# Optimization experiments

Hardware: AMD Instinct MI355X
Metric: run time of the kernel (lower is better)

Reference implementation:

```python
import jax, jax.numpy as jnp
import numpy as np

B, D, ML = 16384, 256, 10
EPS = 1e-6


def setup_inputs() -> dict:
    key = jax.random.key(0)
    ks = jax.random.split(key, 20)
    s = 0.02
    return {
        "O_t": jax.random.normal(ks[0], (B, D), jnp.float32),
        "O_prev": jax.random.normal(ks[1], (B, D), jnp.float32),
        "memory": jax.random.normal(ks[2], (B, ML, D), jnp.float32),
        # weight_mlp: Linear(3 -> D) (see notes re: source bug) + Tanh
        "w_mlp_W": jax.random.normal(ks[3], (D, 3), jnp.float32) * s,
        "w_mlp_b": jnp.zeros((D,), jnp.float32),
        # single-step LSTM (input 2D -> hidden D), torch gate order i,f,g,o
        "lstm_Wih": jax.random.normal(ks[4], (4 * D, 2 * D), jnp.float32) * s,
        "lstm_Whh": jax.random.normal(ks[5], (4 * D, D), jnp.float32) * s,
        "lstm_bih": jnp.zeros((4 * D,), jnp.float32),
        "lstm_bhh": jnp.zeros((4 * D,), jnp.float32),
        "q_W": jax.random.normal(ks[6], (D, D), jnp.float32) * s,
        "q_b": jnp.zeros((D,), jnp.float32),
        "k_W": jax.random.normal(ks[7], (D, D), jnp.float32) * s,
        "k_b": jnp.zeros((D,), jnp.float32),
        "v_W": jax.random.normal(ks[8], (D, D), jnp.float32) * s,
        "v_b": jnp.zeros((D,), jnp.float32),
        "z_W": jax.random.normal(ks[9], (D, 2 * D), jnp.float32) * s,
        "z_b": jnp.zeros((D,), jnp.float32),
        "r_W": jax.random.normal(ks[10], (D, 2 * D), jnp.float32) * s,
        "r_b": jnp.zeros((D,), jnp.float32),
        "h_W": jax.random.normal(ks[11], (D, 2 * D), jnp.float32) * s,
        "h_b": jnp.zeros((D,), jnp.float32),
    }


def _dltc(O_t, O_prev, memory, w_mlp_W, w_mlp_b, lstm_Wih, lstm_Whh,
          lstm_bih, lstm_bhh, q_W, q_b, k_W, k_b, v_W, v_b,
          z_W, z_b, r_W, r_b, h_W, h_b):
    d = O_t.shape[1]
    # --- dynamic frame weighting ---
    n_t = jnp.linalg.norm(O_t, axis=1, keepdims=True)            # [B,1]
    n_p = jnp.linalg.norm(O_prev, axis=1, keepdims=True)         # [B,1]
    rho_delta = jnp.linalg.norm(O_t - O_prev, axis=1, keepdims=True)
    rho_assoc = jnp.sum(O_t * O_prev, axis=1, keepdims=True) / (n_t * n_p + EPS)
    wi = jnp.concatenate([n_t, rho_delta, rho_assoc], axis=1)    # [B,3]
    W_t = (jnp.tanh(wi @ w_mlp_W.T + w_mlp_b) + 1.0) * 0.5       # [B,D]
    O_t_weighted = O_t * W_t
    # --- single-step LSTM with h0=c0=0 ---
    x = jnp.concatenate([O_prev, O_t_weighted], axis=1)          # [B,2D]
    gates = x @ lstm_Wih.T + lstm_bih + lstm_bhh                 # h0=0 => no Whh term
    i_g, f_g, g_g, o_g = jnp.split(gates, 4, axis=1)
    c = jax.nn.sigmoid(i_g) * jnp.tanh(g_g)                      # f*c0 = 0
    O_t_prime = jax.nn.sigmoid(o_g) * jnp.tanh(c)                # [B,D]
    # --- tiny attention over memory ---
    Q = O_t_prime @ q_W.T + q_b                                  # [B,D]
    K = memory @ k_W.T + k_b                                     # [B,M,D]
    V = memory @ v_W.T + v_b
    scores = jnp.einsum('bd,bmd->bm', Q, K) / jnp.sqrt(jnp.float32(d))
    attn = jax.nn.softmax(scores, axis=-1)                       # [B,M]
    O_up = jnp.einsum('bm,bmd->bd', attn, V)                     # [B,D]
    # --- GRU-style gated memory update ---
    O_up_b = jnp.broadcast_to(O_up[:, None, :], memory.shape)    # [B,M,D]
    mem_cat = jnp.concatenate([memory, O_up_b], axis=2)          # [B,M,2D]
    z_t = jax.nn.sigmoid(mem_cat @ z_W.T + z_b)
    r_t = jax.nn.sigmoid(mem_cat @ r_W.T + r_b)
    m_tilde = jnp.tanh(jnp.concatenate([r_t * memory, O_up_b], axis=2) @ h_W.T + h_b)
    memory_new = z_t * memory + (1.0 - z_t) * m_tilde
    memory_new = jnp.concatenate([memory_new[:, 1:], O_up[:, None, :]], axis=1)
    return O_up, memory_new, O_up, W_t


def reference(O_t, O_prev, memory, w_mlp_W, w_mlp_b, lstm_Wih, lstm_Whh,
              lstm_bih, lstm_bhh, q_W, q_b, k_W, k_b, v_W, v_b,
              z_W, z_b, r_W, r_b, h_W, h_b):
    return _dltc(O_t, O_prev, memory, w_mlp_W, w_mlp_b, lstm_Wih, lstm_Whh,
                 lstm_bih, lstm_bhh, q_W, q_b, k_W, k_b, v_W, v_b,
                 z_W, z_b, r_W, r_b, h_W, h_b)
```

## Files before the change

kernel.cpp:

```cpp
#include <hip/hip_runtime.h>

#define BB 16384
#define DD 256

typedef _Float16 f16;
typedef _Float16 h8 __attribute__((ext_vector_type(8)));
typedef float v4f __attribute__((ext_vector_type(4)));

#define MFMA(a,b,c) __builtin_amdgcn_mfma_f32_16x16x32_f16((a),(b),(c),0,0,0)

__device__ __forceinline__ float sigm(float x){ return 1.0f/(1.0f + __expf(-x)); }
__device__ __forceinline__ float tanh_f(float x){ float e = __expf(2.0f*x); return 1.0f - 2.0f/(e + 1.0f); }

__device__ __forceinline__ h8 ldsA(const f16* s, int row, int stride, int k0){
  int g = (k0 >> 3) ^ (row & 7);
  return *reinterpret_cast<const h8*>(s + row*stride + g*8);
}

__global__ __launch_bounds__(512) void k0_convert(
    const float* __restrict__ Wih, const float* __restrict__ vW,
    const float* __restrict__ zW, const float* __restrict__ rW, const float* __restrict__ hW,
    f16* __restrict__ wih16, f16* __restrict__ wv16, f16* __restrict__ w2,
    f16* __restrict__ wzr1, f16* __restrict__ wh1)
{
  int idx = blockIdx.x*512 + threadIdx.x;
  if (idx < 393216){
    int j = idx >> 9, k = idx & 511;
    int sj = (j < 256) ? j : j + 256;
    wih16[idx] = (f16)Wih[sj*512 + k];
    return;
  }
  idx -= 393216;
  if (idx < 65536){ wv16[idx] = (f16)vW[idx]; return; }
  idx -= 65536;
  if (idx < 196608){
    int j = idx >> 8, k = idx & 255;
    float v = (j < 256) ? zW[j*512 + 256 + k]
            : (j < 512) ? rW[(j-256)*512 + 256 + k]
                        : hW[(j-512)*512 + 256 + k];
    w2[idx] = (f16)v;
    return;
  }
  idx -= 196608;
  if (idx < 131072){
    int j = idx >> 8, k = idx & 255;
    wzr1[idx] = (f16)((j < 256) ? zW[j*512 + k] : rW[(j-256)*512 + k]);
    return;
  }
  idx -= 131072;
  {
    int j = idx >> 8, k = idx & 255;
    wh1[idx] = (f16)hW[j*512 + k];
  }
}

__global__ __launch_bounds__(256) void k0_wqkt(const float* __restrict__ qW, const float* __restrict__ kW,
                                               f16* __restrict__ wqkt)
{
  int d = blockIdx.x, e = threadIdx.x;
  float acc = 0.f;
  for (int j = 0; j < 256; ++j) acc += qW[j*256 + e] * kW[j*256 + d];
  wqkt[d*256 + e] = (f16)acc;
}

__global__ __launch_bounds__(256) void k0_misc(const float* __restrict__ qW, const float* __restrict__ kW,
                                               const float* __restrict__ qb, const float* __restrict__ kb,
                                               float* __restrict__ bqk, float* __restrict__ u, float* __restrict__ c0)
{
  int e = threadIdx.x;
  float a = 0.f, b = 0.f;
  for (int j = 0; j < 256; ++j){ a += qb[j]*kW[j*256 + e]; b += kb[j]*qW[j*256 + e]; }
  bqk[e] = a; u[e] = b;
  if (e == 0){ float c = 0.f; for (int j = 0; j < 256; ++j) c += qb[j]*kb[j]; c0[0] = c; }
}

__global__ __launch_bounds__(512) void k1_frontend(
    const float* __restrict__ O_t, const float* __restrict__ O_prev,
    const float* __restrict__ mlpW, const float* __restrict__ mlpB,
    const float* __restrict__ bih, const float* __restrict__ bhh,
    const f16* __restrict__ wih16, const f16* __restrict__ wqkt,
    const float* __restrict__ bqk, const float* __restrict__ u, const float* __restrict__ c0,
    float* __restrict__ wt_out, float* __restrict__ Qk, float* __restrict__ sQ)
{
  __shared__ f16 xs[32*512];
  __shared__ f16 o1[32*256];
  const int t   = threadIdx.x;
  const int b0  = blockIdx.x * 32;
  const int r   = t >> 4, sub = t & 15;
  const int b   = b0 + r;

  {
    float ot[16], op[16];
    float stt = 0.f, spp = 0.f, stp = 0.f;
    const float* pt = O_t    + b*DD + sub*16;
    const float* pp = O_prev + b*DD + sub*16;
#pragma unroll
    for (int i = 0; i < 4; ++i){
      float4 a = *reinterpret_cast<const float4*>(pt + i*4);
      float4 c = *reinterpret_cast<const float4*>(pp + i*4);
      ot[i*4+0]=a.x; ot[i*4+1]=a.y; ot[i*4+2]=a.z; ot[i*4+3]=a.w;
      op[i*4+0]=c.x; op[i*4+1]=c.y; op[i*4+2]=c.z; op[i*4+3]=c.w;
      stt += a.x*a.x + a.y*a.y + a.z*a.z + a.w*a.w;
      spp += c.x*c.x + c.y*c.y + c.z*c.z + c.w*c.w;
      stp += a.x*c.x + a.y*c.y + a.z*c.z + a.w*c.w;
    }
#pragma unroll
    for (int off = 8; off >= 1; off >>= 1){
      stt += __shfl_xor(stt, off);
      spp += __shfl_xor(spp, off);
      stp += __shfl_xor(stp, off);
    }
    float n_t = sqrtf(stt), n_p = sqrtf(spp);
    float r_d = sqrtf(fmaxf(stt - 2.f*stp + spp, 0.f));
    float r_a = stp / (n_t*n_p + 1e-6f);

    h8 h0, h1;
#pragma unroll
    for (int j = 0; j < 8; ++j){ h0[j] = (f16)op[j]; h1[j] = (f16)op[8+j]; }
    *reinterpret_cast<h8*>(&xs[r*512 + (((sub*2  ) ^ (r&7)))*8]) = h0;
    *reinterpret_cast<h8*>(&xs[r*512 + (((sub*2+1) ^ (r&7)))*8]) = h1;

    float wts[16];
#pragma unroll
    for (int i = 0; i < 16; ++i){
      int d = sub*16 + i;
      float xv = mlpW[d*3+0]*n_t + mlpW[d*3+1]*r_d + mlpW[d*3+2]*r_a + mlpB[d];
      wts[i] = 0.5f*(tanh_f(xv) + 1.0f);
    }
#pragma unroll
    for (int i = 0; i < 16; i += 4){
      float4 v; v.x=wts[i]; v.y=wts[i+1]; v.z=wts[i+2]; v.w=wts[i+3];
      *reinterpret_cast<float4*>(wt_out + (size_t)b*DD + sub*16 + i) = v;
    }
    h8 u0, u1;
#pragma unroll
    for (int j = 0; j < 8; ++j){ u0[j] = (f16)(ot[j]*wts[j]); u1[j] = (f16)(ot[8+j]*wts[8+j]); }
    *reinterpret_cast<h8*>(&xs[r*512 + (((32 + sub*2  ) ^ (r&7)))*8]) = u0;
    *reinterpret_cast<h8*>(&xs[r*512 + (((32 + sub*2+1) ^ (r&7)))*8]) = u1;
  }
  __syncthreads();

  const int w = t >> 6, l = t & 63;
  const int lr = l & 15, lk = l >> 4;

  {
    v4f acc[3][2][2];
#pragma unroll
    for (int g = 0; g < 3; ++g)
#pragma unroll
      for (int dt = 0; dt < 2; ++dt)
#pragma unroll
        for (int mt = 0; mt < 2; ++mt) acc[g][dt][mt] = (v4f){0.f,0.f,0.f,0.f};

    for (int ks = 0; ks < 16; ++ks){
      h8 A0 = ldsA(xs, lr,      512, ks*32 + lk*8);
      h8 A1 = ldsA(xs, 16 + lr, 512, ks*32 + lk*8);
#pragma unroll
      for (int dt = 0; dt < 2; ++dt){
        const int dbase = (w*2 + dt)*16;
#pragma unroll
        for (int g = 0; g < 3; ++g){
          const int jrow = g*256 + dbase + lr;
          h8 Bf = *reinterpret_cast<const h8*>(wih16 + jrow*512 + ks*32 + lk*8);
          acc[g][dt][0] = MFMA(A0, Bf, acc[g][dt][0]);
          acc[g][dt][1] = MFMA(A1, Bf, acc[g][dt][1]);
        }
      }
    }
#pragma unroll
    for (int dt = 0; dt < 2; ++dt){
      const int d  = (w*2 + dt)*16 + lr;
      const float bi = bih[d]       + bhh[d];
      const float bg = bih[512 + d] + bhh[512 + d];
      const float bo = bih[768 + d] + bhh[768 + d];
#pragma unroll
      for (int mt = 0; mt < 2; ++mt){
#pragma unroll
        for (int q = 0; q < 4; ++q){
          const int row = mt*16 + lk*4 + q;
          float iv = sigm(acc[0][dt][mt][q] + bi);
          float gv = tanh_f(acc[1][dt][mt][q] + bg);
          float ov = sigm(acc[2][dt][mt][q] + bo);
          float o  = ov * tanh_f(iv*gv);
          int g = ((d >> 3) ^ (row & 7));
          o1[row*256 + g*8 + (d & 7)] = (f16)o;
        }
      }
    }
  }
  __syncthreads();

  {
    float s = 0.f;
#pragma unroll
    for (int i = 0; i < 16; ++i){
      int dd = sub*16 + i;
      int g = ((dd >> 3) ^ (r & 7));
      s += (float)o1[r*256 + g*8 + (dd & 7)] * u[dd];
    }
#pragma unroll
    for (int off = 8; off >= 1; off >>= 1) s += __shfl_xor(s, off);
    if (sub == 0) sQ[b] = s + c0[0];
  }

  {
    v4f acc[2][2];
#pragma unroll
    for (int nt = 0; nt < 2; ++nt)
#pragma unroll
      for (int mt = 0; mt < 2; ++mt) acc[nt][mt] = (v4f){0.f,0.f,0.f,0.f};

    for (int ks = 0; ks < 8; ++ks){
      h8 A0 = ldsA(o1, lr,      256, ks*32 + lk*8);
      h8 A1 = ldsA(o1, 16 + lr, 256, ks*32 + lk*8);
#pragma unroll
      for (int nt = 0; nt < 2; ++nt){
        const int dcol = (w*2 + nt)*16 + lr;
        h8 Bf = *reinterpret_cast<const h8*>(wqkt + dcol*256 + ks*32 + lk*8);
        acc[nt][0] = MFMA(A0, Bf, acc[nt][0]);
        acc[nt][1] = MFMA(A1, Bf, acc[nt][1]);
      }
    }
#pragma unroll
    for (int nt = 0; nt < 2; ++nt){
      const int dcol = (w*2 + nt)*16 + lr;
      const float bq = bqk[dcol];
#pragma unroll
      for (int mt = 0; mt < 2; ++mt){
#pragma unroll
        for (int q = 0; q < 4; ++q){
          const int row = mt*16 + lk*4 + q;
          Qk[(size_t)(b0 + row)*DD + dcol] = acc[nt][mt][q] + bq;
        }
      }
    }
  }
}

__global__ __launch_bounds__(512) void k2a_attn(
    const float* __restrict__ mem, const float* __restrict__ Qk, const float* __restrict__ sQ,
    const f16* __restrict__ wv16, const float* __restrict__ v_b,
    const f16* __restrict__ w2, float* __restrict__ out, f16* __restrict__ z2r2h2)
{
  extern __shared__ char smem[];
  f16*   ms     = (f16*)  (smem);
  float* qks    = (float*)(smem + 81920);
  float* scores = (float*)(smem + 98304);
  float* attns  = (float*)(smem + 98944);
  f16*   mbar   = (f16*)  (smem + 99584);
  f16*   oup    = (f16*)  (smem + 107776);

  const int t  = threadIdx.x;
  const int b0 = blockIdx.x * 16;
  const int sub = t & 15;

  {
    const float4* src = reinterpret_cast<const float4*>(Qk + (size_t)b0*DD);
    float4* dst = reinterpret_cast<float4*>(qks);
    dst[t] = src[t];
    dst[t + 512] = src[t + 512];
  }
  __syncthreads();

  for (int p = 0; p < 5; ++p){
    const int rl = p*32 + (t >> 4);
    const int bl = rl / 10;
    const float* srcp = mem + ((size_t)(b0*10 + rl))*DD + sub*16;
    const float* qrow = qks + bl*DD + sub*16;
    float s = 0.f;
    f16 hv[16];
#pragma unroll
    for (int i = 0; i < 4; ++i){
      float4 v = *reinterpret_cast<const float4*>(srcp + i*4);
      float4 q = *reinterpret_cast<const float4*>(qrow + i*4);
      s += v.x*q.x + v.y*q.y + v.z*q.z + v.w*q.w;
      hv[i*4+0]=(f16)v.x; hv[i*4+1]=(f16)v.y; hv[i*4+2]=(f16)v.z; hv[i*4+3]=(f16)v.w;
    }
    h8 h0, h1;
#pragma unroll
    for (int j = 0; j < 8; ++j){ h0[j]=hv[j]; h1[j]=hv[8+j]; }
    *reinterpret_cast<h8*>(&ms[rl*256 + (((sub*2  ) ^ (rl&7)))*8]) = h0;
    *reinterpret_cast<h8*>(&ms[rl*256 + (((sub*2+1) ^ (rl&7)))*8]) = h1;
#pragma unroll
    for (int off = 8; off >= 1; off >>= 1) s += __shfl_xor(s, off);
    if (sub == 0) scores[rl] = s;
  }
  __syncthreads();

  if (t < 16){
    const float sq = sQ[b0 + t];
    float e[10]; float mx = -1e30f;
#pragma unroll
    for (int m = 0; m < 10; ++m){ e[m] = (scores[t*10 + m] + sq)*0.0625f; mx = fmaxf(mx, e[m]); }
    float ss = 0.f;
#pragma unroll
    for (int m = 0; m < 10; ++m){ e[m] = __expf(e[m] - mx); ss += e[m]; }
    float inv = 1.f/ss;
#pragma unroll
    for (int m = 0; m < 10; ++m) attns[t*10 + m] = e[m]*inv;
  }
  __syncthreads();

  {
    const int rr = t >> 5;
    const int s5 = t & 31;
    float a[8];
#pragma unroll
    for (int i = 0; i < 8; ++i) a[i] = 0.f;
#pragma unroll
    for (int m = 0; m < 10; ++m){
      const int row = rr*10 + m;
      const float wg = attns[row];
      h8 h = *reinterpret_cast<const h8*>(&ms[row*256 + ((s5 ^ (row&7)))*8]);
#pragma unroll
      for (int i = 0; i < 8; ++i) a[i] += wg*(float)h[i];
    }
    h8 hb;
#pragma unroll
    for (int i = 0; i < 8; ++i) hb[i] = (f16)a[i];
    *reinterpret_cast<h8*>(&mbar[rr*256 + ((s5 ^ (rr&7)))*8]) = hb;
  }
  __syncthreads();

  const int w = t >> 6, l = t & 63, lr = l & 15, lk = l >> 4;

  {
    v4f acc[2]; acc[0] = (v4f){0.f,0.f,0.f,0.f}; acc[1] = (v4f){0.f,0.f,0.f,0.f};
    for (int ks = 0; ks < 8; ++ks){
      h8 A = ldsA(mbar, lr, 256, ks*32 + lk*8);
#pragma unroll
      for (int nt = 0; nt < 2; ++nt){
        const int col = (w*2 + nt)*16 + lr;
        h8 Bf = *reinterpret_cast<const h8*>(wv16 + col*256 + ks*32 + lk*8);
        acc[nt] = MFMA(A, Bf, acc[nt]);
      }
    }
#pragma unroll
    for (int nt = 0; nt < 2; ++nt){
      const int col = (w*2 + nt)*16 + lr;
      const float vb = v_b[col];
#pragma unroll
      for (int q = 0; q < 4; ++q){
        const int row = lk*4 + q;
        const int bb = b0 + row;
        float v = acc[nt][q] + vb;
        out[(size_t)bb*DD + col] = v;
        out[(size_t)11*BB*DD + (size_t)bb*DD + col] = v;
        out[(size_t)BB*DD + ((size_t)bb*10 + 9)*DD + col] = v;
        int g = ((col >> 3) ^ (row & 7));
        oup[row*256 + g*8 + (col & 7)] = (f16)v;
      }
    }
  }
  __syncthreads();

  {
    v4f acc[6];
#pragma unroll
    for (int j = 0; j < 6; ++j) acc[j] = (v4f){0.f,0.f,0.f,0.f};
    for (int ks = 0; ks < 8; ++ks){
      h8 A = ldsA(oup, lr, 256, ks*32 + lk*8);
#pragma unroll
      for (int j = 0; j < 6; ++j){
        const int ntg = w*6 + j;
        h8 Bf = *reinterpret_cast<const h8*>(w2 + (ntg*16 + lr)*256 + ks*32 + lk*8);
        acc[j] = MFMA(A, Bf, acc[j]);
      }
    }
#pragma unroll
    for (int j = 0; j < 6; ++j){
      const int colg = (w*6 + j)*16 + lr;
#pragma unroll
      for (int q = 0; q < 4; ++q){
        const int row = lk*4 + q;
        z2r2h2[((size_t)(b0 + row))*768 + colg] = (f16)acc[j][q];
      }
    }
  }
}

__global__ __launch_bounds__(512) void k2b_update(
    const float* __restrict__ mem, const f16* __restrict__ wzr1, const f16* __restrict__ wh1,
    const f16* __restrict__ z2r2h2, const float* __restrict__ z_b, const float* __restrict__ r_b,
    const float* __restrict__ h_b, float* __restrict__ out1)
{
  extern __shared__ char smem[];
  f16* ms = (f16*)smem;
  f16* a2 = (f16*)(smem + 40960);

  const int t  = threadIdx.x;
  const int b0 = blockIdx.x * 8;
  const int sub = t & 15;

  for (int p = 0; p < 3; ++p){
    const int rl = p*32 + (t >> 4);
    if (rl < 80){
      const float* srcp = mem + ((size_t)(b0*10 + rl))*DD + sub*16;
      f16 hv[16];
#pragma unroll
      for (int i = 0; i < 4; ++i){
        float4 v = *reinterpret_cast<const float4*>(srcp + i*4);
        hv[i*4+0]=(f16)v.x; hv[i*4+1]=(f16)v.y; hv[i*4+2]=(f16)v.z; hv[i*4+3]=(f16)v.w;
      }
      h8 h0, h1;
#pragma unroll
      for (int j = 0; j < 8; ++j){ h0[j]=hv[j]; h1[j]=hv[8+j]; }
      *reinterpret_cast<h8*>(&ms[rl*256 + (((sub*2  ) ^ (rl&7)))*8]) = h0;
      *reinterpret_cast<h8*>(&ms[rl*256 + (((sub*2+1) ^ (rl&7)))*8]) = h1;
    }
  }
  __syncthreads();

  const int w = t >> 6, l = t & 63, lr = l & 15, lk = l >> 4;
  float zreg[5][2][4];

  {
    v4f acc[5][2];
#pragma unroll
    for (int mt = 0; mt < 5; ++mt){ acc[mt][0]=(v4f){0.f,0.f,0.f,0.f}; acc[mt][1]=(v4f){0.f,0.f,0.f,0.f}; }
    for (int ks = 0; ks < 8; ++ks){
      h8 A[5];
#pragma unroll
      for (int mt = 0; mt < 5; ++mt) A[mt] = ldsA(ms, mt*16 + lr, 256, ks*32 + lk*8);
#pragma unroll
      for (int nt = 0; nt < 2; ++nt){
        const int jrow = (w*2 + nt)*16 + lr;
        h8 Bf = *reinterpret_cast<const h8*>(wzr1 + jrow*256 + ks*32 + lk*8);
#pragma unroll
        for (int mt = 0; mt < 5; ++mt) acc[mt][nt] = MFMA(A[mt], Bf, acc[mt][nt]);
      }
    }
#pragma unroll
    for (int mt = 0; mt < 5; ++mt)
#pragma unroll
      for (int nt = 0; nt < 2; ++nt){
        const int col = (w*2 + nt)*16 + lr;
#pragma unroll
        for (int q = 0; q < 4; ++q){
          const int row = mt*16 + lk*4 + q;
          const int bb = b0 + row/10;
          float x = acc[mt][nt][q] + (float)z2r2h2[(size_t)bb*768 + col] + z_b[col];
          zreg[mt][nt][q] = sigm(x);
        }
      }
  }

  {
    v4f acc[5][2];
#pragma unroll
    for (int mt = 0; mt < 5; ++mt){ acc[mt][0]=(v4f){0.f,0.f,0.f,0.f}; acc[mt][1]=(v4f){0.f,0.f,0.f,0.f}; }
    for (int ks = 0; ks < 8; ++ks){
      h8 A[5];
#pragma unroll
      for (int mt = 0; mt < 5; ++mt) A[mt] = ldsA(ms, mt*16 + lr, 256, ks*32 + lk*8);
#pragma unroll
      for (int nt = 0; nt < 2; ++nt){
        const int jrow = 256 + (w*2 + nt)*16 + lr;
        h8 Bf = *reinterpret_cast<const h8*>(wzr1 + jrow*256 + ks*32 + lk*8);
#pragma unroll
        for (int mt = 0; mt < 5; ++mt) acc[mt][nt] = MFMA(A[mt], Bf, acc[mt][nt]);
      }
    }
#pragma unroll
    for (int mt = 0; mt < 5; ++mt)
#pragma unroll
      for (int nt = 0; nt < 2; ++nt){
        const int col = (w*2 + nt)*16 + lr;
#pragma unroll
        for (int q = 0; q < 4; ++q){
          const int row = mt*16 + lk*4 + q;
          const int bb = b0 + row/10;
          float x = acc[mt][nt][q] + (float)z2r2h2[(size_t)bb*768 + 256 + col] + r_b[col];
          float rv = sigm(x);
          int g = ((col >> 3) ^ (row & 7));
          float mv = (float)ms[row*256 + g*8 + (col & 7)];
          a2[row*256 + g*8 + (col & 7)] = (f16)(rv*mv);
        }
      }
  }
  __syncthreads();

  {
    v4f acc[5][2];
#pragma unroll
    for (int mt = 0; mt < 5; ++mt){ acc[mt][0]=(v4f){0.f,0.f,0.f,0.f}; acc[mt][1]=(v4f){0.f,0.f,0.f,0.f}; }
    for (int ks = 0; ks < 8; ++ks){
      h8 A[5];
#pragma unroll
      for (int mt = 0; mt < 5; ++mt) A[mt] = ldsA(a2, mt*16 + lr, 256, ks*32 + lk*8);
#pragma unroll
      for (int nt = 0; nt < 2; ++nt){
        const int jrow = (w*2 + nt)*16 + lr;
        h8 Bf = *reinterpret_cast<const h8*>(wh1 + jrow*256 + ks*32 + lk*8);
#pragma unroll
        for (int mt = 0; mt < 5; ++mt) acc[mt][nt] = MFMA(A[mt], Bf, acc[mt][nt]);
      }
    }
#pragma unroll
    for (int mt = 0; mt < 5; ++mt)
#pragma unroll
      for (int nt = 0; nt < 2; ++nt){
        const int col = (w*2 + nt)*16 + lr;
#pragma unroll
        for (int q = 0; q < 4; ++q){
          const int row = mt*16 + lk*4 + q;
          const int bl = row/10;
          const int m  = row - bl*10;
          const int bb = b0 + bl;
          float mtld = tanh_f(acc[mt][nt][q] + (float)z2r2h2[(size_t)bb*768 + 512 + col] + h_b[col]);
          int g = ((col >> 3) ^ (row & 7));
          float mv = (float)ms[row*256 + g*8 + (col & 7)];
          float z = zreg[mt][nt][q];
          float res = z*mv + (1.f - z)*mtld;
          if (m > 0) out1[((size_t)bb*10 + (m-1))*DD + col] = res;
        }
      }
  }
}

extern "C" void kernel_launch(void* const* d_in, const int* in_sizes, int n_in,
                              void* d_out, int out_size, void* d_ws, size_t ws_size,
                              hipStream_t stream)
{
  (void)in_sizes; (void)n_in; (void)out_size; (void)ws_size;

  const float* O_t    = (const float*)d_in[0];
  const float* O_prev = (const float*)d_in[1];
  const float* mem    = (const float*)d_in[2];
  const float* mlpW   = (const float*)d_in[3];
  const float* mlpB   = (const float*)d_in[4];
  const float* Wih    = (const float*)d_in[5];
  const float* bih    = (const float*)d_in[7];
  const float* bhh    = (const float*)d_in[8];
  const float* qW     = (const float*)d_in[9];
  const float* qb     = (const float*)d_in[10];
  const float* kW     = (const float*)d_in[11];
  const float* kb     = (const float*)d_in[12];
  const float* vW     = (const float*)d_in[13];
  const float* vb     = (const float*)d_in[14];
  const float* zW     = (const float*)d_in[15];
  const float* zb     = (const float*)d_in[16];
  const float* rW     = (const float*)d_in[17];
  const float* rb     = (const float*)d_in[18];
  const float* hW     = (const float*)d_in[19];
  const float* hb     = (const float*)d_in[20];

  char* ws = (char*)d_ws;
  f16*   wih16 = (f16*)  (ws + 0);
  f16*   wqkt  = (f16*)  (ws + 786432);
  f16*   wv16  = (f16*)  (ws + 917504);
  f16*   w2    = (f16*)  (ws + 1048576);
  f16*   wzr1  = (f16*)  (ws + 1441792);
  f16*   wh1   = (f16*)  (ws + 1703936);
  float* bqk   = (float*)(ws + 1835008);
  float* u     = (float*)(ws + 1836032);
  float* c0    = (float*)(ws + 1837056);
  float* Qk    = (float*)(ws + 2097152);
  float* sQ    = (float*)(ws + 18874368);
  f16*   z2r2h2= (f16*)  (ws + 18939904);

  float* out    = (float*)d_out;
  float* wt_out = out + (size_t)12*BB*DD;
  float* out1   = out + (size_t)BB*DD;

  hipFuncSetAttribute((const void*)k2a_attn,  hipFuncAttributeMaxDynamicSharedMemorySize, 116224);
  hipFuncSetAttribute((const void*)k2b_update, hipFuncAttributeMaxDynamicSharedMemorySize, 81920);

  k0_convert<<<dim3(1664), dim3(512), 0, stream>>>(Wih, vW, zW, rW, hW, wih16, wv16, w2, wzr1, wh1);
  k0_wqkt  <<<dim3(256),  dim3(256), 0, stream>>>(qW, kW, wqkt);
  k0_misc  <<<dim3(1),    dim3(256), 0, stream>>>(qW, kW, qb, kb, bqk, u, c0);
  k1_frontend<<<dim3(512), dim3(512), 0, stream>>>(O_t, O_prev, mlpW, mlpB, bih, bhh,
                                                   wih16, wqkt, bqk, u, c0, wt_out, Qk, sQ);
  k2a_attn <<<dim3(1024), dim3(512), 116224, stream>>>(mem, Qk, sQ, wv16, vb, w2, out, z2r2h2);
  k2b_update<<<dim3(2048), dim3(512), 81920, stream>>>(mem, wzr1, wh1, z2r2h2, zb, rb, hb, out1);
}
```

Baseline: 879.8 us.

## Fuse attention and GRU memory update into one pipelined kernel

Merges the attention kernel and the gated-update kernel into a single kernel. Each block handles four groups of 8 batches, double-buffering the fp16 memory tile in LDS and prefetching the next group's memory rows into registers while computing. This removes the second read of the large memory tensor and the z2r2h2 global round trip. Outputs are staged through LDS for coalesced float4 stores, and a few inner loops are fully unrolled. The cost is higher LDS use per block (about 152KB), which limits occupancy, plus heavy register pressure from the prefetch buffers and accumulators, and fewer blocks overall.

```diff
diff --git a/kernel.cpp b/kernel.cpp
--- a/kernel.cpp
+++ b/kernel.cpp
@@ -2,6 +2,8 @@
 
 #define BB 16384
 #define DD 256
+#define GPB 4
+#define TBG 8
 
 typedef _Float16 f16;
 typedef _Float16 h8 __attribute__((ext_vector_type(8)));
@@ -15,6 +17,13 @@
 __device__ __forceinline__ h8 ldsA(const f16* s, int row, int stride, int k0){
   int g = (k0 >> 3) ^ (row & 7);
   return *reinterpret_cast<const h8*>(s + row*stride + g*8);
+}
+
+__device__ __forceinline__ void bar_lds(){
+  __builtin_amdgcn_sched_barrier(0);
+  asm volatile("s_waitcnt lgkmcnt(0)" ::: "memory");
+  __builtin_amdgcn_s_barrier();
+  __builtin_amdgcn_sched_barrier(0);
 }
 
 __global__ __launch_bounds__(512) void k0_convert(
@@ -152,6 +161,7 @@
 #pragma unroll
         for (int mt = 0; mt < 2; ++mt) acc[g][dt][mt] = (v4f){0.f,0.f,0.f,0.f};
 
+#pragma unroll
     for (int ks = 0; ks < 16; ++ks){
       h8 A0 = ldsA(xs, lr,      512, ks*32 + lk*8);
       h8 A1 = ldsA(xs, 16 + lr, 512, ks*32 + lk*8);
@@ -210,6 +220,7 @@
 #pragma unroll
       for (int mt = 0; mt < 2; ++mt) acc[nt][mt] = (v4f){0.f,0.f,0.f,0.f};
 
+#pragma unroll
     for (int ks = 0; ks < 8; ++ks){
       h8 A0 = ldsA(o1, lr,      256, ks*32 + lk*8);
       h8 A1 = ldsA(o1, 16 + lr, 256, ks*32 + lk*8);
@@ -237,284 +248,344 @@
   }
 }
 
-__global__ __launch_bounds__(512) void k2a_attn(
+
+__device__ __forceinline__ void issue_grp(float4* pf, const float* __restrict__ mem, int gb0, int t){
+  const float* basep = mem + (size_t)gb0*10*DD;
+  {
+    const float* p = basep + (t>>4)*DD + (t&15)*16;
+    pf[0] = reinterpret_cast<const float4*>(p)[0];
+    pf[1] = reinterpret_cast<const float4*>(p)[1];
+    pf[2] = reinterpret_cast<const float4*>(p)[2];
+    pf[3] = reinterpret_cast<const float4*>(p)[3];
+  }
+  {
+    const int s = t + 512;
+    const float* p = basep + (s>>4)*DD + (s&15)*16;
+    pf[4] = reinterpret_cast<const float4*>(p)[0];
+    pf[5] = reinterpret_cast<const float4*>(p)[1];
+    pf[6] = reinterpret_cast<const float4*>(p)[2];
+    pf[7] = reinterpret_cast<const float4*>(p)[3];
+  }
+  if (t < 256){
+    const int s = t + 1024;
+    const float* p = basep + (s>>4)*DD + (s&15)*16;
+    pf[8]  = reinterpret_cast<const float4*>(p)[0];
+    pf[9]  = reinterpret_cast<const float4*>(p)[1];
+    pf[10] = reinterpret_cast<const float4*>(p)[2];
+    pf[11] = reinterpret_cast<const float4*>(p)[3];
+  }
+}
+
+__device__ __forceinline__ void conv_slot(f16* __restrict__ buf, const float4* pf, int s,
+    const float* __restrict__ Qk, int gb0, float* __restrict__ scoresL)
+{
+  const int rl = s >> 4, cs = s & 15;
+  const float* qrow = Qk + (size_t)(gb0 + rl/10)*DD + cs*16;
+  float sum = 0.f;
+  h8 h0, h1;
+  {
+    float4 v = pf[0]; float4 q = reinterpret_cast<const float4*>(qrow)[0];
+    sum += v.x*q.x + v.y*q.y + v.z*q.z + v.w*q.w;
+    h0[0]=(f16)v.x; h0[1]=(f16)v.y; h0[2]=(f16)v.z; h0[3]=(f16)v.w;
+  }
+  {
+    float4 v = pf[1]; float4 q = reinterpret_cast<const float4*>(qrow)[1];
+    sum += v.x*q.x + v.y*q.y + v.z*q.z + v.w*q.w;
+    h0[4]=(f16)v.x; h0[5]=(f16)v.y; h0[6]=(f16)v.z; h0[7]=(f16)v.w;
+  }
+  {
+    float4 v = pf[2]; float4 q = reinterpret_cast<const float4*>(qrow)[2];
+    sum += v.x*q.x + v.y*q.y + v.z*q.z + v.w*q.w;
+    h1[0]=(f16)v.x; h1[1]=(f16)v.y; h1[2]=(f16)v.z; h1[3]=(f16)v.w;
+  }
+  {
+    float4 v = pf[3]; float4 q = reinterpret_cast<const float4*>(qrow)[3];
+    sum += v.x*q.x + v.y*q.y + v.z*q.z + v.w*q.w;
+    h1[4]=(f16)v.x; h1[5]=(f16)v.y; h1[6]=(f16)v.z; h1[7]=(f16)v.w;
+  }
+  *reinterpret_cast<h8*>(buf + rl*256 + (((cs*2  ) ^ (rl&7)))*8) = h0;
+  *reinterpret_cast<h8*>(buf + rl*256 + (((cs*2+1) ^ (rl&7)))*8) = h1;
+#pragma unroll
+  for (int off = 8; off >= 1; off >>= 1) sum += __shfl_xor(sum, off);
+  if (cs == 0) scoresL[rl] = sum;
+}
+
+__global__ __launch_bounds__(512) void k2_fused(
     const float* __restrict__ mem, const float* __restrict__ Qk, const float* __restrict__ sQ,
-    const f16* __restrict__ wv16, const float* __restrict__ v_b,
-    const f16* __restrict__ w2, float* __restrict__ out, f16* __restrict__ z2r2h2)
+    const f16* __restrict__ wv16, const float* __restrict__ v_b, const f16* __restrict__ w2,
+    const f16* __restrict__ wzr1, const f16* __restrict__ wh1,
+    const float* __restrict__ z_b, const float* __restrict__ r_b, const float* __restrict__ h_b,
+    float* __restrict__ out, float* __restrict__ out1)
 {
   extern __shared__ char smem[];
-  f16*   ms     = (f16*)  (smem);
-  float* qks    = (float*)(smem + 81920);
-  float* scores = (float*)(smem + 98304);
-  float* attns  = (float*)(smem + 98944);
-  f16*   mbar   = (f16*)  (smem + 99584);
-  f16*   oup    = (f16*)  (smem + 107776);
-
-  const int t  = threadIdx.x;
-  const int b0 = blockIdx.x * 16;
-  const int sub = t & 15;
-
-  {
-    const float4* src = reinterpret_cast<const float4*>(Qk + (size_t)b0*DD);
-    float4* dst = reinterpret_cast<float4*>(qks);
-    dst[t] = src[t];
-    dst[t + 512] = src[t + 512];
-  }
-  __syncthreads();
-
-  for (int p = 0; p < 5; ++p){
-    const int rl = p*32 + (t >> 4);
-    const int bl = rl / 10;
-    const float* srcp = mem + ((size_t)(b0*10 + rl))*DD + sub*16;
-    const float* qrow = qks + bl*DD + sub*16;
-    float s = 0.f;
-    f16 hv[16];
-#pragma unroll
-    for (int i = 0; i < 4; ++i){
-      float4 v = *reinterpret_cast<const float4*>(srcp + i*4);
-      float4 q = *reinterpret_cast<const float4*>(qrow + i*4);
-      s += v.x*q.x + v.y*q.y + v.z*q.z + v.w*q.w;
-      hv[i*4+0]=(f16)v.x; hv[i*4+1]=(f16)v.y; hv[i*4+2]=(f16)v.z; hv[i*4+3]=(f16)v.w;
-    }
-    h8 h0, h1;
-#pragma unroll
-    for (int j = 0; j < 8; ++j){ h0[j]=hv[j]; h1[j]=hv[8+j]; }
-    *reinterpret_cast<h8*>(&ms[rl*256 + (((sub*2  ) ^ (rl&7)))*8]) = h0;
-    *reinterpret_cast<h8*>(&ms[rl*256 + (((sub*2+1) ^ (rl&7)))*8]) = h1;
-#pragma unroll
-    for (int off = 8; off >= 1; off >>= 1) s += __shfl_xor(s, off);
-    if (sub == 0) scores[rl] = s;
-  }
-  __syncthreads();
-
-  if (t < 16){
-    const float sq = sQ[b0 + t];
-    float e[10]; float mx = -1e30f;
-#pragma unroll
-    for (int m = 0; m < 10; ++m){ e[m] = (scores[t*10 + m] + sq)*0.0625f; mx = fmaxf(mx, e[m]); }
-    float ss = 0.f;
-#pragma unroll
-    for (int m = 0; m < 10; ++m){ e[m] = __expf(e[m] - mx); ss += e[m]; }
-    float inv = 1.f/ss;
-#pragma unroll
-    for (int m = 0; m < 10; ++m) attns[t*10 + m] = e[m]*inv;
-  }
-  __syncthreads();
-
-  {
-    const int rr = t >> 5;
-    const int s5 = t & 31;
-    float a[8];
-#pragma unroll
-    for (int i = 0; i < 8; ++i) a[i] = 0.f;
-#pragma unroll
-    for (int m = 0; m < 10; ++m){
-      const int row = rr*10 + m;
-      const float wg = attns[row];
-      h8 h = *reinterpret_cast<const h8*>(&ms[row*256 + ((s5 ^ (row&7)))*8]);
-#pragma unroll
-      for (int i = 0; i < 8; ++i) a[i] += wg*(float)h[i];
-    }
-    h8 hb;
-#pragma unroll
-    for (int i = 0; i < 8; ++i) hb[i] = (f16)a[i];
-    *reinterpret_cast<h8*>(&mbar[rr*256 + ((s5 ^ (rr&7)))*8]) = hb;
-  }
-  __syncthreads();
-
+  f16*   msA     = (f16*)  (smem);
+  f16*   msB     = (f16*)  (smem + 40960);
+  f16*   a2      = (f16*)  (smem + 81920);
+  float* stg     = (float*)(smem + 81920);
+  f16*   zrh     = (f16*)  (smem + 122880);
+  float* oupf    = (float*)(smem + 135168);
+  f16*   mbar    = (f16*)  (smem + 143360);
+  f16*   oup16   = (f16*)  (smem + 147456);
+  float* scoresL = (float*)(smem + 151552);
+  float* attnL   = (float*)(smem + 151872);
+
+  const int t = threadIdx.x;
   const int w = t >> 6, l = t & 63, lr = l & 15, lk = l >> 4;
-
-  {
-    v4f acc[2]; acc[0] = (v4f){0.f,0.f,0.f,0.f}; acc[1] = (v4f){0.f,0.f,0.f,0.f};
-    for (int ks = 0; ks < 8; ++ks){
-      h8 A = ldsA(mbar, lr, 256, ks*32 + lk*8);
+  const int blk_b0 = blockIdx.x * (GPB*TBG);
+
+  float4 pf[12];
+  issue_grp(pf, mem, blk_b0, t);
+
+  for (int g = 0; g < GPB; ++g){
+    const int gb0 = blk_b0 + g*TBG;
+    f16* buf = (g & 1) ? msB : msA;
+
+    conv_slot(buf, pf + 0, t,        Qk, gb0, scoresL);
+    conv_slot(buf, pf + 4, t + 512,  Qk, gb0, scoresL);
+    if (t < 256) conv_slot(buf, pf + 8, t + 1024, Qk, gb0, scoresL);
+    bar_lds();
+
+    if (g + 1 < GPB) issue_grp(pf, mem, blk_b0 + (g+1)*TBG, t);
+
+    if (t < TBG){
+      const float sq = sQ[gb0 + t];
+      float e[10]; float mx = -1e30f;
+#pragma unroll
+      for (int m = 0; m < 10; ++m){ e[m] = (scoresL[t*10 + m] + sq)*0.0625f; mx = fmaxf(mx, e[m]); }
+      float ss = 0.f;
+#pragma unroll
+      for (int m = 0; m < 10; ++m){ e[m] = __expf(e[m] - mx); ss += e[m]; }
+      float inv = 1.f/ss;
+#pragma unroll
+      for (int m = 0; m < 10; ++m) attnL[t*10 + m] = e[m]*inv;
+    }
+    bar_lds();
+
+    if (t < 256){
+      const int rr = t >> 5, gg = t & 31;
+      float a[8];
+#pragma unroll
+      for (int i = 0; i < 8; ++i) a[i] = 0.f;
+#pragma unroll
+      for (int m = 0; m < 10; ++m){
+        const int row = rr*10 + m;
+        const float wg = attnL[row];
+        h8 h = *reinterpret_cast<const h8*>(buf + row*256 + ((gg ^ (row&7)))*8);
+#pragma unroll
+        for (int i = 0; i < 8; ++i) a[i] += wg*(float)h[i];
+      }
+      h8 hb;
+#pragma unroll
+      for (int i = 0; i < 8; ++i) hb[i] = (f16)a[i];
+      *reinterpret_cast<h8*>(mbar + rr*256 + ((gg ^ (rr&7)))*8) = hb;
+    }
+    bar_lds();
+
+    {
+      v4f accO[2]; accO[0] = (v4f){0.f,0.f,0.f,0.f}; accO[1] = (v4f){0.f,0.f,0.f,0.f};
+#pragma unroll
+      for (int ks = 0; ks < 8; ++ks){
+        const int k0 = ks*32 + lk*8;
+        h8 A = ldsA(mbar, lr, 256, k0);
+#pragma unroll
+        for (int nt = 0; nt < 2; ++nt){
+          const int col = (w*2 + nt)*16 + lr;
+          h8 Bf = *reinterpret_cast<const h8*>(wv16 + (size_t)col*256 + k0);
+          accO[nt] = MFMA(A, Bf, accO[nt]);
+        }
+      }
 #pragma unroll
       for (int nt = 0; nt < 2; ++nt){
         const int col = (w*2 + nt)*16 + lr;
-        h8 Bf = *reinterpret_cast<const h8*>(wv16 + col*256 + ks*32 + lk*8);
-        acc[nt] = MFMA(A, Bf, acc[nt]);
-      }
-    }
-#pragma unroll
-    for (int nt = 0; nt < 2; ++nt){
-      const int col = (w*2 + nt)*16 + lr;
-      const float vb = v_b[col];
-#pragma unroll
-      for (int q = 0; q < 4; ++q){
-        const int row = lk*4 + q;
-        const int bb = b0 + row;
-        float v = acc[nt][q] + vb;
-        out[(size_t)bb*DD + col] = v;
-        out[(size_t)11*BB*DD + (size_t)bb*DD + col] = v;
-        out[(size_t)BB*DD + ((size_t)bb*10 + 9)*DD + col] = v;
-        int g = ((col >> 3) ^ (row & 7));
-        oup[row*256 + g*8 + (col & 7)] = (f16)v;
-      }
-    }
-  }
-  __syncthreads();
-
-  {
-    v4f acc[6];
-#pragma unroll
-    for (int j = 0; j < 6; ++j) acc[j] = (v4f){0.f,0.f,0.f,0.f};
-    for (int ks = 0; ks < 8; ++ks){
-      h8 A = ldsA(oup, lr, 256, ks*32 + lk*8);
+        const float vb = v_b[col];
+#pragma unroll
+        for (int q = 0; q < 4; ++q){
+          const int row = lk*4 + q;
+          if (row < 8){
+            float val = accO[nt][q] + vb;
+            oupf[row*256 + col] = val;
+            oup16[row*256 + ((col>>3) ^ (row&7))*8 + (col&7)] = (f16)val;
+          }
+        }
+      }
+    }
+    bar_lds();
+
+    {
+      const int row = t >> 6, c4 = t & 63;
+      float4 v = *reinterpret_cast<const float4*>(oupf + row*256 + c4*4);
+      const size_t bb = (size_t)gb0 + row;
+      *reinterpret_cast<float4*>(out + bb*DD + c4*4) = v;
+      *reinterpret_cast<float4*>(out + (size_t)11*BB*DD + bb*DD + c4*4) = v;
+      *reinterpret_cast<float4*>(out1 + (bb*10 + 9)*DD + c4*4) = v;
+    }
+
+    {
+      v4f accZ[6];
+#pragma unroll
+      for (int j = 0; j < 6; ++j) accZ[j] = (v4f){0.f,0.f,0.f,0.f};
+#pragma unroll
+      for (int ks = 0; ks < 8; ++ks){
+        const int k0 = ks*32 + lk*8;
+        h8 A = ldsA(oup16, lr, 256, k0);
+#pragma unroll
+        for (int j = 0; j < 6; ++j){
+          const int colg = (w*6 + j)*16 + lr;
+          h8 Bf = *reinterpret_cast<const h8*>(w2 + (size_t)colg*256 + k0);
+          accZ[j] = MFMA(A, Bf, accZ[j]);
+        }
+      }
 #pragma unroll
       for (int j = 0; j < 6; ++j){
-        const int ntg = w*6 + j;
-        h8 Bf = *reinterpret_cast<const h8*>(w2 + (ntg*16 + lr)*256 + ks*32 + lk*8);
-        acc[j] = MFMA(A, Bf, acc[j]);
-      }
-    }
-#pragma unroll
-    for (int j = 0; j < 6; ++j){
-      const int colg = (w*6 + j)*16 + lr;
-#pragma unroll
-      for (int q = 0; q < 4; ++q){
-        const int row = lk*4 + q;
-        z2r2h2[((size_t)(b0 + row))*768 + colg] = (f16)acc[j][q];
-      }
-    }
-  }
-}
-
-__global__ __launch_bounds__(512) void k2b_update(
-    const float* __restrict__ mem, const f16* __restrict__ wzr1, const f16* __restrict__ wh1,
-    const f16* __restrict__ z2r2h2, const float* __restrict__ z_b, const float* __restrict__ r_b,
-    const float* __restrict__ h_b, float* __restrict__ out1)
-{
-  extern __shared__ char smem[];
-  f16* ms = (f16*)smem;
-  f16* a2 = (f16*)(smem + 40960);
-
-  const int t  = threadIdx.x;
-  const int b0 = blockIdx.x * 8;
-  const int sub = t & 15;
-
-  for (int p = 0; p < 3; ++p){
-    const int rl = p*32 + (t >> 4);
-    if (rl < 80){
-      const float* srcp = mem + ((size_t)(b0*10 + rl))*DD + sub*16;
-      f16 hv[16];
-#pragma unroll
-      for (int i = 0; i < 4; ++i){
-        float4 v = *reinterpret_cast<const float4*>(srcp + i*4);
-        hv[i*4+0]=(f16)v.x; hv[i*4+1]=(f16)v.y; hv[i*4+2]=(f16)v.z; hv[i*4+3]=(f16)v.w;
-      }
-      h8 h0, h1;
-#pragma unroll
-      for (int j = 0; j < 8; ++j){ h0[j]=hv[j]; h1[j]=hv[8+j]; }
-      *reinterpret_cast<h8*>(&ms[rl*256 + (((sub*2  ) ^ (rl&7)))*8]) = h0;
-      *reinterpret_cast<h8*>(&ms[rl*256 + (((sub*2+1) ^ (rl&7)))*8]) = h1;
-    }
-  }
-  __syncthreads();
-
-  const int w = t >> 6, l = t & 63, lr = l & 15, lk = l >> 4;
-  float zreg[5][2][4];
-
-  {
-    v4f acc[5][2];
-#pragma unroll
-    for (int mt = 0; mt < 5; ++mt){ acc[mt][0]=(v4f){0.f,0.f,0.f,0.f}; acc[mt][1]=(v4f){0.f,0.f,0.f,0.f}; }
-    for (int ks = 0; ks < 8; ++ks){
-      h8 A[5];
-#pragma unroll
-      for (int mt = 0; mt < 5; ++mt) A[mt] = ldsA(ms, mt*16 + lr, 256, ks*32 + lk*8);
-#pragma unroll
-      for (int nt = 0; nt < 2; ++nt){
-        const int jrow = (w*2 + nt)*16 + lr;
-        h8 Bf = *reinterpret_cast<const h8*>(wzr1 + jrow*256 + ks*32 + lk*8);
-#pragma unroll
-        for (int mt = 0; mt < 5; ++mt) acc[mt][nt] = MFMA(A[mt], Bf, acc[mt][nt]);
-      }
-    }
-#pragma unroll
-    for (int mt = 0; mt < 5; ++mt)
-#pragma unroll
-      for (int nt = 0; nt < 2; ++nt){
-        const int col = (w*2 + nt)*16 + lr;
+        const int colg = (w*6 + j)*16 + lr;
 #pragma unroll
         for (int q = 0; q < 4; ++q){
-          const int row = mt*16 + lk*4 + q;
-          const int bb = b0 + row/10;
-          float x = acc[mt][nt][q] + (float)z2r2h2[(size_t)bb*768 + col] + z_b[col];
-          zreg[mt][nt][q] = sigm(x);
-        }
-      }
-  }
-
-  {
-    v4f acc[5][2];
-#pragma unroll
-    for (int mt = 0; mt < 5; ++mt){ acc[mt][0]=(v4f){0.f,0.f,0.f,0.f}; acc[mt][1]=(v4f){0.f,0.f,0.f,0.f}; }
-    for (int ks = 0; ks < 8; ++ks){
-      h8 A[5];
-#pragma unroll
-      for (int mt = 0; mt < 5; ++mt) A[mt] = ldsA(ms, mt*16 + lr, 256, ks*32 + lk*8);
-#pragma unroll
-      for (int nt = 0; nt < 2; ++nt){
-        const int jrow = 256 + (w*2 + nt)*16 + lr;
-        h8 Bf = *reinterpret_cast<const h8*>(wzr1 + jrow*256 + ks*32 + lk*8);
-#pragma unroll
-        for (int mt = 0; mt < 5; ++mt) acc[mt][nt] = MFMA(A[mt], Bf, acc[mt][nt]);
-      }
-    }
-#pragma unroll
-    for (int mt = 0; mt < 5; ++mt)
-#pragma unroll
-      for (int nt = 0; nt < 2; ++nt){
-        const int col = (w*2 + nt)*16 + lr;
-#pragma unroll
-        for (int q = 0; q < 4; ++q){
-          const int row = mt*16 + lk*4 + q;
-          const int bb = b0 + row/10;
-          float x = acc[mt][nt][q] + (float)z2r2h2[(size_t)bb*768 + 256 + col] + r_b[col];
-          float rv = sigm(x);
-          int g = ((col >> 3) ^ (row & 7));
-          float mv = (float)ms[row*256 + g*8 + (col & 7)];
-          a2[row*256 + g*8 + (col & 7)] = (f16)(rv*mv);
-        }
-      }
-  }
-  __syncthreads();
-
-  {
-    v4f acc[5][2];
-#pragma unroll
-    for (int mt = 0; mt < 5; ++mt){ acc[mt][0]=(v4f){0.f,0.f,0.f,0.f}; acc[mt][1]=(v4f){0.f,0.f,0.f,0.f}; }
-    for (int ks = 0; ks < 8; ++ks){
-      h8 A[5];
-#pragma unroll
-      for (int mt = 0; mt < 5; ++mt) A[mt] = ldsA(a2, mt*16 + lr, 256, ks*32 + lk*8);
-#pragma unroll
-      for (int nt = 0; nt < 2; ++nt){
-        const int jrow = (w*2 + nt)*16 + lr;
-        h8 Bf = *reinterpret_cast<const h8*>(wh1 + jrow*256 + ks*32 + lk*8);
-#pragma unroll
-        for (int mt = 0; mt < 5; ++mt) acc[mt][nt] = MFMA(A[mt], Bf, acc[mt][nt]);
-      }
-    }
-#pragma unroll
-    for (int mt = 0; mt < 5; ++mt)
-#pragma unroll
-      for (int nt = 0; nt < 2; ++nt){
-        const int col = (w*2 + nt)*16 + lr;
-#pragma unroll
-        for (int q = 0; q < 4; ++q){
-          const int row = mt*16 + lk*4 + q;
-          const int bl = row/10;
-          const int m  = row - bl*10;
-          const int bb = b0 + bl;
-          float mtld = tanh_f(acc[mt][nt][q] + (float)z2r2h2[(size_t)bb*768 + 512 + col] + h_b[col]);
-          int g = ((col >> 3) ^ (row & 7));
-          float mv = (float)ms[row*256 + g*8 + (col & 7)];
-          float z = zreg[mt][nt][q];
-          float res = z*mv + (1.f - z)*mtld;
-          if (m > 0) out1[((size_t)bb*10 + (m-1))*DD + col] = res;
-        }
-      }
+          const int row = lk*4 + q;
+          if (row < 8) zrh[row*768 + colg] = (f16)accZ[j][q];
+        }
+      }
+    }
+    bar_lds();
+
+    float zreg[5][2][4];
+    float zmv[5][2][4];
+
+    {
+      v4f acc[5][2];
+#pragma unroll
+      for (int mt = 0; mt < 5; ++mt){ acc[mt][0]=(v4f){0.f,0.f,0.f,0.f}; acc[mt][1]=(v4f){0.f,0.f,0.f,0.f}; }
+#pragma unroll
+      for (int ks = 0; ks < 8; ++ks){
+        const int k0 = ks*32 + lk*8;
+        h8 A[5];
+#pragma unroll
+        for (int mt = 0; mt < 5; ++mt) A[mt] = ldsA(buf, mt*16 + lr, 256, k0);
+#pragma unroll
+        for (int nt = 0; nt < 2; ++nt){
+          h8 Bf = *reinterpret_cast<const h8*>(wzr1 + (size_t)((w*2 + nt)*16 + lr)*256 + k0);
+#pragma unroll
+          for (int mt = 0; mt < 5; ++mt) acc[mt][nt] = MFMA(A[mt], Bf, acc[mt][nt]);
+        }
+      }
+#pragma unroll
+      for (int mt = 0; mt < 5; ++mt)
+#pragma unroll
+        for (int nt = 0; nt < 2; ++nt){
+          const int col = (w*2 + nt)*16 + lr;
+#pragma unroll
+          for (int q = 0; q < 4; ++q){
+            const int row = mt*16 + lk*4 + q;
+            const int bl = row/10;
+            float x = acc[mt][nt][q] + (float)zrh[bl*768 + col] + z_b[col];
+            zreg[mt][nt][q] = sigm(x);
+          }
+        }
+    }
+
+    {
+      v4f acc[5][2];
+#pragma unroll
+      for (int mt = 0; mt < 5; ++mt){ acc[mt][0]=(v4f){0.f,0.f,0.f,0.f}; acc[mt][1]=(v4f){0.f,0.f,0.f,0.f}; }
+#pragma unroll
+      for (int ks = 0; ks < 8; ++ks){
+        const int k0 = ks*32 + lk*8;
+        h8 A[5];
+#pragma unroll
+        for (int mt = 0; mt < 5; ++mt) A[mt] = ldsA(buf, mt*16 + lr, 256, k0);
+#pragma unroll
+        for (int nt = 0; nt < 2; ++nt){
+          h8 Bf = *reinterpret_cast<const h8*>(wzr1 + (size_t)(256 + (w*2 + nt)*16 + lr)*256 + k0);
+#pragma unroll
+          for (int mt = 0; mt < 5; ++mt) acc[mt][nt] = MFMA(A[mt], Bf, acc[mt][nt]);
+        }
+      }
+#pragma unroll
+      for (int mt = 0; mt < 5; ++mt)
+#pragma unroll
+        for (int nt = 0; nt < 2; ++nt){
+          const int col = (w*2 + nt)*16 + lr;
+#pragma unroll
+          for (int q = 0; q < 4; ++q){
+            const int row = mt*16 + lk*4 + q;
+            const int bl = row/10;
+            float x = acc[mt][nt][q] + (float)zrh[bl*768 + 256 + col] + r_b[col];
+            float rv = sigm(x);
+            float mvv = (float)buf[row*256 + ((col>>3) ^ (row&7))*8 + (col&7)];
+            zmv[mt][nt][q] = zreg[mt][nt][q] * mvv;
+            a2[row*256 + ((col>>3) ^ (row&7))*8 + (col&7)] = (f16)(rv*mvv);
+          }
+        }
+    }
+    bar_lds();
+
+    {
+      v4f acc[5][2];
+#pragma unroll
+      for (int mt = 0; mt < 5; ++mt){ acc[mt][0]=(v4f){0.f,0.f,0.f,0.f}; acc[mt][1]=(v4f){0.f,0.f,0.f,0.f}; }
+#pragma unroll
+      for (int ks = 0; ks < 8; ++ks){
+        const int k0 = ks*32 + lk*8;
+        h8 A[5];
+#pragma unroll
+        for (int mt = 0; mt < 5; ++mt) A[mt] = ldsA(a2, mt*16 + lr, 256, k0);
+#pragma unroll
+        for (int nt = 0; nt < 2; ++nt){
+          h8 Bf = *reinterpret_cast<const h8*>(wh1 + (size_t)((w*2 + nt)*16 + lr)*256 + k0);
+#pragma unroll
+          for (int mt = 0; mt < 5; ++mt) acc[mt][nt] = MFMA(A[mt], Bf, acc[mt][nt]);
+        }
+      }
+#pragma unroll
+      for (int mt = 0; mt < 5; ++mt)
+#pragma unroll
+        for (int nt = 0; nt < 2; ++nt){
+          const int col = (w*2 + nt)*16 + lr;
+#pragma unroll
+          for (int q = 0; q < 4; ++q){
+            const int row = mt*16 + lk*4 + q;
+            const int bl = row/10;
+            float mtld = tanh_f(acc[mt][nt][q] + (float)zrh[bl*768 + 512 + col] + h_b[col]);
+            zmv[mt][nt][q] = zmv[mt][nt][q] + (1.f - zreg[mt][nt][q])*mtld;
+          }
+        }
+    }
+    bar_lds();
+
+#pragma unroll
+    for (int rd = 0; rd < 3; ++rd){
+      const int rbase = rd*32;
+#pragma unroll
+      for (int mi = 0; mi < 2; ++mi){
+        const int mt = rd*2 + mi;
+        if (mt < 5){
+#pragma unroll
+          for (int nt = 0; nt < 2; ++nt){
+            const int col = (w*2 + nt)*16 + lr;
+#pragma unroll
+            for (int q = 0; q < 4; ++q){
+              const int row = mt*16 + lk*4 + q;
+              stg[(row - rbase)*256 + col] = zmv[mt][nt][q];
+            }
+          }
+        }
+      }
+      bar_lds();
+      const int nf4 = (rd < 2) ? 2048 : 1024;
+      for (int p = 0; p < 4; ++p){
+        const int f = p*512 + t;
+        if (f < nf4){
+          const int rowl = f >> 6;
+          const int grow = rbase + rowl;
+          const int bl = grow/10;
+          const int m  = grow - bl*10;
+          if (m){
+            float4 v = *reinterpret_cast<const float4*>(stg + (size_t)f*4);
+            *reinterpret_cast<float4*>(out1 + ((size_t)(gb0 + bl)*10 + (m-1))*DD + (f & 63)*4) = v;
+          }
+        }
+      }
+      bar_lds();
+    }
   }
 }
 
@@ -557,20 +628,18 @@
   float* c0    = (float*)(ws + 1837056);
   float* Qk    = (float*)(ws + 2097152);
   float* sQ    = (float*)(ws + 18874368);
-  f16*   z2r2h2= (f16*)  (ws + 18939904);
 
   float* out    = (float*)d_out;
   float* wt_out = out + (size_t)12*BB*DD;
   float* out1   = out + (size_t)BB*DD;
 
-  hipFuncSetAttribute((const void*)k2a_attn,  hipFuncAttributeMaxDynamicSharedMemorySize, 116224);
-  hipFuncSetAttribute((const void*)k2b_update, hipFuncAttributeMaxDynamicSharedMemorySize, 81920);
+  hipFuncSetAttribute((const void*)k2_fused, hipFuncAttributeMaxDynamicSharedMemorySize, 152192);
 
   k0_convert<<<dim3(1664), dim3(512), 0, stream>>>(Wih, vW, zW, rW, hW, wih16, wv16, w2, wzr1, wh1);
   k0_wqkt  <<<dim3(256),  dim3(256), 0, stream>>>(qW, kW, wqkt);
   k0_misc  <<<dim3(1),    dim3(256), 0, stream>>>(qW, kW, qb, kb, bqk, u, c0);
   k1_frontend<<<dim3(512), dim3(512), 0, stream>>>(O_t, O_prev, mlpW, mlpB, bih, bhh,
                                                    wih16, wqkt, bqk, u, c0, wt_out, Qk, sQ);
-  k2a_attn <<<dim3(1024), dim3(512), 116224, stream>>>(mem, Qk, sQ, wv16, vb, w2, out, z2r2h2);
-  k2b_update<<<dim3(2048), dim3(512), 81920, stream>>>(mem, wzr1, wh1, z2r2h2, zb, rb, hb, out1);
-}
+  k2_fused <<<dim3(512), dim3(512), 152192, stream>>>(mem, Qk, sQ, wv16, vb, w2, wzr1, wh1,
+                                                      zb, rb, hb, out, out1);
+}
```

Measured after the change: 1.634 ms. 1.86x slower.
